# Kernel tuning notes

Measured on AMD Instinct MI355X. Metric: run time of the kernel, lower is better.

Reference implementation:

```python
import jax, jax.numpy as jnp
import numpy as np

N_HEAD = 8
D_MODEL = 128  # per-head dim == d_model in this 'interpretable' MHA
B, S = 2, 2048
LN_EPS = 1e-3  # keras LayerNormalization default epsilon


def setup_inputs() -> dict:
    key = jax.random.key(0)
    ks = jax.random.split(key, 8)
    sc = 1.0 / np.sqrt(D_MODEL)
    q = jax.random.normal(ks[0], (B, S, D_MODEL), jnp.float32)
    k = jax.random.normal(ks[1], (B, S, D_MODEL), jnp.float32)
    v = jax.random.normal(ks[2], (B, S, D_MODEL), jnp.float32)
    # multiplicative causal mask (lower-triangular ones), broadcast over B,H
    mask = jnp.tril(jnp.ones((S, S), jnp.float32))[None, None, :, :]
    Wq = jax.random.normal(ks[3], (D_MODEL, N_HEAD * D_MODEL), jnp.float32) * sc
    Wk = jax.random.normal(ks[4], (D_MODEL, N_HEAD * D_MODEL), jnp.float32) * sc
    Wv = jax.random.normal(ks[5], (D_MODEL, N_HEAD * D_MODEL), jnp.float32) * sc
    Wo = jax.random.normal(ks[6], (N_HEAD * D_MODEL, D_MODEL), jnp.float32) * sc
    gamma = jnp.ones((D_MODEL,), jnp.float32)
    beta = jnp.zeros((D_MODEL,), jnp.float32)
    return {"q": q, "k": k, "v": v, "mask": mask, "Wq": Wq, "Wk": Wk,
            "Wv": Wv, "Wo": Wo, "gamma": gamma, "beta": beta}


def reference(q, k, v, mask, Wq, Wk, Wv, Wo, gamma, beta):
    b = q.shape[0]
    # projections -> [B, H, S, D]
    def split_heads(x):
        return x.reshape(b, -1, N_HEAD, D_MODEL).transpose(0, 2, 1, 3)
    qs = split_heads(q @ Wq)
    ks_ = split_heads(k @ Wk)
    vs = split_heads(v @ Wv)
    scores = jnp.einsum('bhqd,bhkd->bhqk', qs, ks_) / jnp.sqrt(jnp.float32(D_MODEL))
    scores = scores * mask  # multiplicative mask (NOT additive -inf)
    attn = jax.nn.softmax(scores, axis=-1)
    # dropout layers are identity at inference
    out = jnp.einsum('bhqk,bhkd->bhqd', attn, vs)
    out = out.transpose(0, 2, 1, 3).reshape(b, -1, N_HEAD * D_MODEL)
    out = out @ Wo
    # keras LayerNorm (axis=-1, eps=1e-3)
    mu = jnp.mean(out, axis=-1, keepdims=True)
    var = jnp.var(out, axis=-1, keepdims=True)
    out = (out - mu) * jax.lax.rsqrt(var + LN_EPS) * gamma + beta
    return out
```

## Files before the change

kernel.cpp:

```cpp
#include <hip/hip_runtime.h>
#include <math.h>

#define B 2
#define S 2048
#define H 8
#define D 128
#define DM 1024
#define BH 16

typedef unsigned short u16;
typedef __attribute__((ext_vector_type(8))) short bf16x8;
typedef __attribute__((ext_vector_type(8))) unsigned short u16x8;
typedef __attribute__((ext_vector_type(4))) float f32x4;

__device__ __forceinline__ float bf2f(u16 x) {
    union { unsigned u; float f; } c; c.u = ((unsigned)x) << 16; return c.f;
}
__device__ __forceinline__ u16 f2bf(float f) {
    union { unsigned u; float f; } c; c.f = f;
    unsigned u = c.u; u += 0x7fffu + ((u >> 16) & 1u);
    return (u16)(u >> 16);
}
__device__ __forceinline__ u16 ftr(float f) {
    union { unsigned u; float f; } c; c.f = f;
    return (u16)(c.u >> 16);
}

#define MFMA16(a, b, c) __builtin_amdgcn_mfma_f32_16x16x32_bf16((a), (b), (c), 0, 0, 0)

__global__ __launch_bounds__(256) void proj_kernel(
    const float* __restrict__ q, const float* __restrict__ k, const float* __restrict__ v,
    const float* __restrict__ Wq, const float* __restrict__ Wk, const float* __restrict__ Wv,
    u16* __restrict__ Qo, u16* __restrict__ Ko, u16* __restrict__ VTo)
{
    __shared__ __align__(16) u16 Xs[128][136];
    __shared__ __align__(16) u16 Wst[128][136];
    int tid = threadIdx.x;
    int m0 = blockIdx.x * 128;
    int by = blockIdx.y;
    int t = by >> 3;
    int col0 = (by & 7) * 128;
    const float* X = (t == 0) ? q : (t == 1) ? k : v;
    const float* W = (t == 0) ? Wq : (t == 1) ? Wk : Wv;

    u16 (*Wtmp)[136] = Xs;
#pragma unroll
    for (int i = 0; i < 16; i++) {
        int e = i * 256 + tid; int kk = e >> 5, n4 = e & 31;
        float4 w4 = *(const float4*)&W[(size_t)kk * DM + col0 + n4 * 4];
        ushort4 p; p.x = ftr(w4.x); p.y = ftr(w4.y); p.z = ftr(w4.z); p.w = ftr(w4.w);
        *(ushort4*)&Wtmp[kk][n4 * 4] = p;
    }
    __syncthreads();
#pragma unroll
    for (int i = 0; i < 8; i++) {
        int e = i * 256 + tid; int kk = e >> 4, n8 = e & 15;
        u16x8 t8 = *(const u16x8*)&Wtmp[kk][n8 * 8];
#pragma unroll
        for (int j0 = 0; j0 < 8; j0++) {
            int j = (j0 + n8) & 7;
            Wst[n8 * 8 + j][kk] = t8[j];
        }
    }
    __syncthreads();
#pragma unroll
    for (int i = 0; i < 16; i++) {
        int e = i * 256 + tid; int r = e >> 5, c4 = e & 31;
        float4 x4 = *(const float4*)&X[(size_t)(m0 + r) * D + c4 * 4];
        ushort4 p; p.x = ftr(x4.x); p.y = ftr(x4.y); p.z = ftr(x4.z); p.w = ftr(x4.w);
        *(ushort4*)&Xs[r][c4 * 4] = p;
    }
    __syncthreads();

    int w = tid >> 6, lane = tid & 63, quad = lane >> 4, ln = lane & 15;
    bf16x8 aX[2][4];
#pragma unroll
    for (int rf = 0; rf < 2; rf++)
#pragma unroll
        for (int ks = 0; ks < 4; ks++)
            aX[rf][ks] = *(const bf16x8*)&Xs[w * 32 + rf * 16 + ln][ks * 32 + quad * 8];

    f32x4 zero = {0.f, 0.f, 0.f, 0.f};
    f32x4 acc[2][8];
#pragma unroll
    for (int rf = 0; rf < 2; rf++)
#pragma unroll
        for (int nt = 0; nt < 8; nt++) acc[rf][nt] = zero;

#pragma unroll
    for (int ks = 0; ks < 4; ks++)
#pragma unroll
        for (int nt = 0; nt < 8; nt++) {
            bf16x8 bW = *(const bf16x8*)&Wst[nt * 16 + ln][ks * 32 + quad * 8];
            acc[0][nt] = MFMA16(aX[0][ks], bW, acc[0][nt]);
            acc[1][nt] = MFMA16(aX[1][ks], bW, acc[1][nt]);
        }

    int hh = col0 >> 7, bb = m0 >> 11, ss0 = m0 & 2047;
    int bh = bb * 8 + hh;
    if (t < 2) {
        u16* O = (t == 0) ? Qo : Ko;
#pragma unroll
        for (int rf = 0; rf < 2; rf++)
#pragma unroll
            for (int nt = 0; nt < 8; nt++)
#pragma unroll
                for (int r = 0; r < 4; r++) {
                    int ss = ss0 + w * 32 + rf * 16 + quad * 4 + r;
                    O[((size_t)bh * S + ss) * D + nt * 16 + ln] = f2bf(acc[rf][nt][r]);
                }
    } else {
        __syncthreads();
        u16 (*Ct)[136] = Xs;
#pragma unroll
        for (int rf = 0; rf < 2; rf++)
#pragma unroll
            for (int nt = 0; nt < 8; nt++)
#pragma unroll
                for (int r = 0; r < 4; r++)
                    Ct[nt * 16 + ln][w * 32 + rf * 16 + quad * 4 + r] = f2bf(acc[rf][nt][r]);
        __syncthreads();
#pragma unroll
        for (int i = 0; i < 8; i++) {
            int e = i * 256 + tid; int dloc = e >> 4, s8 = e & 15;
            *(u16x8*)&VTo[((size_t)bh * D + dloc) * S + ss0 + s8 * 8] =
                *(const u16x8*)&Ct[dloc][s8 * 8];
        }
    }
}

__global__ __launch_bounds__(256) void wot_kernel(
    const float* __restrict__ Wo, u16* __restrict__ WoT)
{
    __shared__ __align__(16) u16 Wl[64][136];
    int tid = threadIdx.x, k0 = blockIdx.x * 64;
#pragma unroll
    for (int i = 0; i < 8; i++) {
        int e = i * 256 + tid; int kk = e >> 5, n4 = e & 31;
        float4 w4 = *(const float4*)&Wo[(size_t)(k0 + kk) * D + n4 * 4];
        ushort4 p; p.x = ftr(w4.x); p.y = ftr(w4.y); p.z = ftr(w4.z); p.w = ftr(w4.w);
        *(ushort4*)&Wl[kk][n4 * 4] = p;
    }
    __syncthreads();
    int n = tid >> 1, kh = tid & 1;
    u16 tmp[32];
#pragma unroll
    for (int j = 0; j < 32; j++) tmp[j] = Wl[kh * 32 + j][n];
#pragma unroll
    for (int j8 = 0; j8 < 4; j8++)
        *(u16x8*)&WoT[(size_t)n * DM + k0 + kh * 32 + j8 * 8] = *(const u16x8*)&tmp[j8 * 8];
}

__global__ __launch_bounds__(128) void chunk_sum_kernel(
    const u16* __restrict__ VT, float* __restrict__ Csum)
{
    int bh = blockIdx.x, c = blockIdx.y, d = threadIdx.x;
    const u16* p = VT + ((size_t)bh * D + d) * S + c * 64;
    float acc = 0.f;
#pragma unroll
    for (int i = 0; i < 8; i++) {
        u16x8 v8 = *(const u16x8*)&p[i * 8];
#pragma unroll
        for (int j = 0; j < 8; j++) acc += bf2f(v8[j]);
    }
    Csum[((size_t)bh * 32 + c) * D + d] = acc;
}

__global__ __launch_bounds__(128) void scan_kernel(
    const float* __restrict__ Csum, float* __restrict__ SufT)
{
    int bh = blockIdx.x, d = threadIdx.x;
    float acc = 0.f;
    for (int c = 31; c >= 0; c--) {
        SufT[((size_t)bh * 32 + c) * D + d] = acc;
        acc += Csum[((size_t)bh * 32 + c) * D + d];
    }
}

__global__ __launch_bounds__(512, 2) void attn_kernel(
    const u16* __restrict__ Qb, const u16* __restrict__ Kb, const u16* __restrict__ VTg,
    const float* __restrict__ SufT, u16* __restrict__ HOb)
{
    __shared__ __align__(16) u16 Qs[2][64][136];
    __shared__ __align__(16) u16 Ks[128][136];
    __shared__ __align__(16) u16 Vt[128][136];
    __shared__ __align__(16) u16 Ps[2][64][136];
    __shared__ float Lred[2][4][64];

    int tid = threadIdx.x;
    int bx = blockIdx.x, bh = blockIdx.y;
    int nhi = (31 - bx) / 2 + 1, nlo = bx / 2 + 1;
    int w = tid >> 6, qt = w >> 2, wq = w & 3, lane = tid & 63, quad = lane >> 4, ln = lane & 15;
    int qb = qt ? bx : (31 - bx);
    int q0 = qb * 64;
    int nq = qt ? nlo : nhi;
    const u16* Qp  = Qb  + (size_t)bh * S * D;
    const u16* Kp  = Kb  + (size_t)bh * S * D;
    const u16* VTp = VTg + (size_t)bh * D * S;

#pragma unroll
    for (int i = 0; i < 4; i++) {
        int e = i * 512 + tid; int r2 = e >> 4, c8 = e & 15;
        int qtt = r2 >> 6, r = r2 & 63;
        int q0s = (qtt ? bx : (31 - bx)) * 64;
        *(u16x8*)&Qs[qtt][r][c8 * 8] = *(const u16x8*)&Qp[(size_t)(q0s + r) * D + c8 * 8];
    }
    __syncthreads();
    bf16x8 aQ[4][4];
#pragma unroll
    for (int rf = 0; rf < 4; rf++)
#pragma unroll
        for (int ks = 0; ks < 4; ks++)
            aQ[rf][ks] = *(const bf16x8*)&Qs[qt][rf * 16 + ln][ks * 32 + quad * 8];

    f32x4 zero = {0.f, 0.f, 0.f, 0.f};
    f32x4 accPV[4][2], acc_l[4];
#pragma unroll
    for (int rf = 0; rf < 4; rf++) { accPV[rf][0] = zero; accPV[rf][1] = zero; acc_l[rf] = zero; }
    bf16x8 bOnes;
#pragma unroll
    for (int j = 0; j < 8; j++) bOnes[j] = (short)0x3F80;
    const float scale = 0.08838834764831845f;

    for (int kt = 0; kt < nhi; kt++) {
        __syncthreads();
        int k0 = kt * 128;
#pragma unroll
        for (int i = 0; i < 4; i++) {
            int e = i * 512 + tid; int r = e >> 4, c8 = e & 15;
            *(u16x8*)&Ks[r][c8 * 8] = *(const u16x8*)&Kp[(size_t)(k0 + r) * D + c8 * 8];
        }
#pragma unroll
        for (int i = 0; i < 4; i++) {
            int e = i * 512 + tid; int dd = e >> 4, c8 = e & 15;
            *(u16x8*)&Vt[dd][c8 * 8] = *(const u16x8*)&VTp[(size_t)dd * S + k0 + c8 * 8];
        }
        __syncthreads();
        bool active = (qt == 0) || (kt < nlo);
        if (active) {
            f32x4 s[4][2];
#pragma unroll
            for (int rf = 0; rf < 4; rf++) { s[rf][0] = zero; s[rf][1] = zero; }
#pragma unroll
            for (int ks = 0; ks < 4; ks++) {
                bf16x8 b0 = *(const bf16x8*)&Ks[wq * 32 + ln][ks * 32 + quad * 8];
                bf16x8 b1 = *(const bf16x8*)&Ks[wq * 32 + 16 + ln][ks * 32 + quad * 8];
#pragma unroll
                for (int rf = 0; rf < 4; rf++) {
                    s[rf][0] = MFMA16(aQ[rf][ks], b0, s[rf][0]);
                    s[rf][1] = MFMA16(aQ[rf][ks], b1, s[rf][1]);
                }
            }
#pragma unroll
            for (int rf = 0; rf < 4; rf++)
#pragma unroll
                for (int ct = 0; ct < 2; ct++) {
                    int col = k0 + wq * 32 + ct * 16 + ln;
                    int rowb = q0 + rf * 16 + quad * 4;
#pragma unroll
                    for (int r = 0; r < 4; r++) {
                        float tv = (col <= rowb + r) ? s[rf][ct][r] : 0.f;
                        float p = __expf(tv * scale);
                        Ps[qt][rf * 16 + quad * 4 + r][wq * 32 + ct * 16 + ln] = f2bf(p);
                    }
                }
        }
        __syncthreads();
        if (active) {
#pragma unroll
            for (int ks = 0; ks < 4; ks++) {
                bf16x8 aP[4];
#pragma unroll
                for (int rf = 0; rf < 4; rf++)
                    aP[rf] = *(const bf16x8*)&Ps[qt][rf * 16 + ln][ks * 32 + quad * 8];
                bf16x8 v0 = *(const bf16x8*)&Vt[wq * 32 + ln][ks * 32 + quad * 8];
                bf16x8 v1 = *(const bf16x8*)&Vt[wq * 32 + 16 + ln][ks * 32 + quad * 8];
                if (ks == wq) {
#pragma unroll
                    for (int rf = 0; rf < 4; rf++) acc_l[rf] = MFMA16(aP[rf], bOnes, acc_l[rf]);
                }
#pragma unroll
                for (int rf = 0; rf < 4; rf++) {
                    accPV[rf][0] = MFMA16(aP[rf], v0, accPV[rf][0]);
                    accPV[rf][1] = MFMA16(aP[rf], v1, accPV[rf][1]);
                }
            }
        }
    }

    __syncthreads();
    if (ln == 0) {
#pragma unroll
        for (int rf = 0; rf < 4; rf++)
#pragma unroll
            for (int r = 0; r < 4; r++)
                Lred[qt][wq][rf * 16 + quad * 4 + r] = acc_l[rf][r];
    }
    __syncthreads();

    int scount = S - nq * 128;
    size_t sufb = (size_t)(bh * 32 + 2 * nq - 1) * D + wq * 32;
    float suf0 = SufT[sufb + ln];
    float suf1 = SufT[sufb + 16 + ln];
    int b = bh >> 3, h = bh & 7;
#pragma unroll
    for (int rf = 0; rf < 4; rf++)
#pragma unroll
        for (int r = 0; r < 4; r++) {
            int row = rf * 16 + quad * 4 + r;
            int srow = q0 + row;
            float l = Lred[qt][0][row] + Lred[qt][1][row] + Lred[qt][2][row] + Lred[qt][3][row]
                      + (float)scount;
            float inv = 1.f / l;
            size_t base = ((size_t)(b * S + srow)) * DM + h * D + wq * 32;
            HOb[base + ln]      = f2bf((accPV[rf][0][r] + suf0) * inv);
            HOb[base + 16 + ln] = f2bf((accPV[rf][1][r] + suf1) * inv);
        }
}

__global__ __launch_bounds__(256) void out_ln_kernel(
    const u16* __restrict__ HOb, const u16* __restrict__ WoT,
    const float* __restrict__ gamma, const float* __restrict__ beta,
    float* __restrict__ out)
{
    __shared__ __align__(16) u16 HOs[16][1048];
    __shared__ float Cs[16][132];
    int tid = threadIdx.x;
    int m0 = blockIdx.x * 16;
    int w = tid >> 6, lane = tid & 63, quad = lane >> 4, ln = lane & 15;
#pragma unroll
    for (int i = 0; i < 8; i++) {
        int e = i * 256 + tid; int r = e >> 7, c8 = e & 127;
        *(u16x8*)&HOs[r][c8 * 8] = *(const u16x8*)&HOb[(size_t)(m0 + r) * DM + c8 * 8];
    }
    __syncthreads();
    f32x4 zero = {0.f, 0.f, 0.f, 0.f};
    f32x4 acc[2] = {zero, zero};
#pragma unroll 4
    for (int ks = 0; ks < 32; ks++) {
        bf16x8 aH = *(const bf16x8*)&HOs[ln][ks * 32 + quad * 8];
        bf16x8 w0 = *(const bf16x8*)&WoT[(size_t)(w * 32 + ln) * DM + ks * 32 + quad * 8];
        bf16x8 w1 = *(const bf16x8*)&WoT[(size_t)(w * 32 + 16 + ln) * DM + ks * 32 + quad * 8];
        acc[0] = MFMA16(aH, w0, acc[0]);
        acc[1] = MFMA16(aH, w1, acc[1]);
    }
#pragma unroll
    for (int ct = 0; ct < 2; ct++)
#pragma unroll
        for (int r = 0; r < 4; r++)
            Cs[quad * 4 + r][w * 32 + ct * 16 + ln] = acc[ct][r];
    __syncthreads();

    int row = tid >> 4, t16 = tid & 15;
    float xv[8], sum = 0.f, sq = 0.f;
#pragma unroll
    for (int j = 0; j < 8; j++) {
        float x = Cs[row][t16 * 8 + j];
        xv[j] = x; sum += x; sq += x * x;
    }
#pragma unroll
    for (int off = 1; off < 16; off <<= 1) {
        sum += __shfl_xor(sum, off);
        sq  += __shfl_xor(sq, off);
    }
    float mu = sum * (1.f / 128.f);
    float var = sq * (1.f / 128.f) - mu * mu;
    float rstd = rsqrtf(var + 1e-3f);
    float o[8];
#pragma unroll
    for (int j = 0; j < 8; j++) {
        int c = t16 * 8 + j;
        o[j] = (xv[j] - mu) * rstd * gamma[c] + beta[c];
    }
    float* op = &out[(size_t)(m0 + row) * D + t16 * 8];
    *(float4*)&op[0] = *(float4*)&o[0];
    *(float4*)&op[4] = *(float4*)&o[4];
}

extern "C" void kernel_launch(void* const* d_in, const int* in_sizes, int n_in,
                              void* d_out, int out_size, void* d_ws, size_t ws_size,
                              hipStream_t stream)
{
    const float* q     = (const float*)d_in[0];
    const float* k     = (const float*)d_in[1];
    const float* v     = (const float*)d_in[2];
    const float* Wq    = (const float*)d_in[4];
    const float* Wk    = (const float*)d_in[5];
    const float* Wv    = (const float*)d_in[6];
    const float* Wo    = (const float*)d_in[7];
    const float* gamma = (const float*)d_in[8];
    const float* beta  = (const float*)d_in[9];

    u16* ws16 = (u16*)d_ws;
    u16* Qb  = ws16;
    u16* Kb  = ws16 + 4194304;
    u16* VT  = ws16 + 8388608;
    u16* HOb = ws16 + 12582912;
    u16* WoT = ws16 + 16777216;
    float* Csum = (float*)((char*)d_ws + 33816576);
    float* SufT = (float*)((char*)d_ws + 34078720);

    wot_kernel<<<16, 256, 0, stream>>>(Wo, WoT);
    proj_kernel<<<dim3(32, 24), 256, 0, stream>>>(q, k, v, Wq, Wk, Wv, Qb, Kb, VT);
    chunk_sum_kernel<<<dim3(BH, 32), 128, 0, stream>>>(VT, Csum);
    scan_kernel<<<BH, 128, 0, stream>>>(Csum, SufT);
    attn_kernel<<<dim3(16, BH), 512, 0, stream>>>(Qb, Kb, VT, SufT, HOb);
    out_ln_kernel<<<256, 256, 0, stream>>>(HOb, WoT, gamma, beta, (float*)d_out);
}
```

Measured before the change: 161.6 us.

## Pretranspose projection weights once and fuse chunk sums into projection kernel

A new prep kernel converts Wq/Wk/Wv to bf16 and transposes them once into global workspace, replacing the Wo-only transpose kernel. Each of the 768 projection blocks then reads its pre-transposed weight tile from global memory instead of rebuilding it in shared memory. The per-64-row V chunk sums are computed in the V projection epilogue from the shared-memory tile, removing the separate chunk_sum kernel launch and its re-read of VT. The cost is loading B-operand fragments straight from global/L2 memory inside the MFMA loop rather than from LDS.

```diff
diff --git a/kernel.cpp b/kernel.cpp
--- a/kernel.cpp
+++ b/kernel.cpp
@@ -28,41 +28,70 @@
 
 #define MFMA16(a, b, c) __builtin_amdgcn_mfma_f32_16x16x32_bf16((a), (b), (c), 0, 0, 0)
 
+__global__ __launch_bounds__(256) void prep_kernel(
+    const float* __restrict__ Wq, const float* __restrict__ Wk, const float* __restrict__ Wv,
+    const float* __restrict__ Wo, u16* __restrict__ WT, u16* __restrict__ WoT)
+{
+    __shared__ __align__(16) u16 Wl[128][132];
+    int tid = threadIdx.x, by = blockIdx.x;
+    if (by < 16) {
+        int k0 = by * 64;
+#pragma unroll
+        for (int i = 0; i < 8; i++) {
+            int e = i * 256 + tid; int kk = e >> 5, n4 = e & 31;
+            float4 w4 = *(const float4*)&Wo[(size_t)(k0 + kk) * D + n4 * 4];
+            ushort4 p; p.x = ftr(w4.x); p.y = ftr(w4.y); p.z = ftr(w4.z); p.w = ftr(w4.w);
+            *(ushort4*)&Wl[kk][n4 * 4] = p;
+        }
+        __syncthreads();
+#pragma unroll
+        for (int i = 0; i < 4; i++) {
+            int e = i * 256 + tid; int n = e >> 3, ko = e & 7;
+            u16x8 g;
+#pragma unroll
+            for (int j = 0; j < 8; j++) g[j] = Wl[ko * 8 + j][n];
+            *(u16x8*)&WoT[(size_t)n * DM + k0 + ko * 8] = g;
+        }
+    } else {
+        int tile = by - 16;
+        int t = tile >> 3, h = tile & 7;
+        const float* W = (t == 0) ? Wq : (t == 1) ? Wk : Wv;
+        int col0 = h * 128;
+#pragma unroll
+        for (int i = 0; i < 16; i++) {
+            int e = i * 256 + tid; int kk = e >> 5, n4 = e & 31;
+            float4 w4 = *(const float4*)&W[(size_t)kk * DM + col0 + n4 * 4];
+            ushort4 p; p.x = ftr(w4.x); p.y = ftr(w4.y); p.z = ftr(w4.z); p.w = ftr(w4.w);
+            *(ushort4*)&Wl[kk][n4 * 4] = p;
+        }
+        __syncthreads();
+        u16* WTt = WT + (size_t)tile * (128 * 128);
+#pragma unroll
+        for (int i = 0; i < 8; i++) {
+            int e = i * 256 + tid; int n = e >> 4, ko = e & 15;
+            u16x8 g;
+#pragma unroll
+            for (int j = 0; j < 8; j++) g[j] = Wl[ko * 8 + j][n];
+            *(u16x8*)&WTt[(size_t)n * 128 + ko * 8] = g;
+        }
+    }
+}
+
 __global__ __launch_bounds__(256) void proj_kernel(
     const float* __restrict__ q, const float* __restrict__ k, const float* __restrict__ v,
-    const float* __restrict__ Wq, const float* __restrict__ Wk, const float* __restrict__ Wv,
-    u16* __restrict__ Qo, u16* __restrict__ Ko, u16* __restrict__ VTo)
+    const u16* __restrict__ WT,
+    u16* __restrict__ Qo, u16* __restrict__ Ko, u16* __restrict__ VTo,
+    float* __restrict__ Csum)
 {
     __shared__ __align__(16) u16 Xs[128][136];
-    __shared__ __align__(16) u16 Wst[128][136];
     int tid = threadIdx.x;
     int m0 = blockIdx.x * 128;
     int by = blockIdx.y;
     int t = by >> 3;
-    int col0 = (by & 7) * 128;
+    int h = by & 7;
     const float* X = (t == 0) ? q : (t == 1) ? k : v;
-    const float* W = (t == 0) ? Wq : (t == 1) ? Wk : Wv;
-
-    u16 (*Wtmp)[136] = Xs;
-#pragma unroll
-    for (int i = 0; i < 16; i++) {
-        int e = i * 256 + tid; int kk = e >> 5, n4 = e & 31;
-        float4 w4 = *(const float4*)&W[(size_t)kk * DM + col0 + n4 * 4];
-        ushort4 p; p.x = ftr(w4.x); p.y = ftr(w4.y); p.z = ftr(w4.z); p.w = ftr(w4.w);
-        *(ushort4*)&Wtmp[kk][n4 * 4] = p;
-    }
-    __syncthreads();
-#pragma unroll
-    for (int i = 0; i < 8; i++) {
-        int e = i * 256 + tid; int kk = e >> 4, n8 = e & 15;
-        u16x8 t8 = *(const u16x8*)&Wtmp[kk][n8 * 8];
-#pragma unroll
-        for (int j0 = 0; j0 < 8; j0++) {
-            int j = (j0 + n8) & 7;
-            Wst[n8 * 8 + j][kk] = t8[j];
-        }
-    }
-    __syncthreads();
+    const u16* WTt = WT + (size_t)(t * 8 + h) * (128 * 128);
+
 #pragma unroll
     for (int i = 0; i < 16; i++) {
         int e = i * 256 + tid; int r = e >> 5, c4 = e & 31;
@@ -88,16 +117,20 @@
         for (int nt = 0; nt < 8; nt++) acc[rf][nt] = zero;
 
 #pragma unroll
-    for (int ks = 0; ks < 4; ks++)
+    for (int ks = 0; ks < 4; ks++) {
+        bf16x8 bW[8];
+#pragma unroll
+        for (int nt = 0; nt < 8; nt++)
+            bW[nt] = *(const bf16x8*)&WTt[(size_t)(nt * 16 + ln) * 128 + ks * 32 + quad * 8];
 #pragma unroll
         for (int nt = 0; nt < 8; nt++) {
-            bf16x8 bW = *(const bf16x8*)&Wst[nt * 16 + ln][ks * 32 + quad * 8];
-            acc[0][nt] = MFMA16(aX[0][ks], bW, acc[0][nt]);
-            acc[1][nt] = MFMA16(aX[1][ks], bW, acc[1][nt]);
-        }
-
-    int hh = col0 >> 7, bb = m0 >> 11, ss0 = m0 & 2047;
-    int bh = bb * 8 + hh;
+            acc[0][nt] = MFMA16(aX[0][ks], bW[nt], acc[0][nt]);
+            acc[1][nt] = MFMA16(aX[1][ks], bW[nt], acc[1][nt]);
+        }
+    }
+
+    int bb = m0 >> 11, ss0 = m0 & 2047;
+    int bh = bb * 8 + h;
     if (t < 2) {
         u16* O = (t == 0) ? Qo : Ko;
 #pragma unroll
@@ -126,44 +159,18 @@
             *(u16x8*)&VTo[((size_t)bh * D + dloc) * S + ss0 + s8 * 8] =
                 *(const u16x8*)&Ct[dloc][s8 * 8];
         }
-    }
-}
-
-__global__ __launch_bounds__(256) void wot_kernel(
-    const float* __restrict__ Wo, u16* __restrict__ WoT)
-{
-    __shared__ __align__(16) u16 Wl[64][136];
-    int tid = threadIdx.x, k0 = blockIdx.x * 64;
-#pragma unroll
-    for (int i = 0; i < 8; i++) {
-        int e = i * 256 + tid; int kk = e >> 5, n4 = e & 31;
-        float4 w4 = *(const float4*)&Wo[(size_t)(k0 + kk) * D + n4 * 4];
-        ushort4 p; p.x = ftr(w4.x); p.y = ftr(w4.y); p.z = ftr(w4.z); p.w = ftr(w4.w);
-        *(ushort4*)&Wl[kk][n4 * 4] = p;
-    }
-    __syncthreads();
-    int n = tid >> 1, kh = tid & 1;
-    u16 tmp[32];
-#pragma unroll
-    for (int j = 0; j < 32; j++) tmp[j] = Wl[kh * 32 + j][n];
-#pragma unroll
-    for (int j8 = 0; j8 < 4; j8++)
-        *(u16x8*)&WoT[(size_t)n * DM + k0 + kh * 32 + j8 * 8] = *(const u16x8*)&tmp[j8 * 8];
-}
-
-__global__ __launch_bounds__(128) void chunk_sum_kernel(
-    const u16* __restrict__ VT, float* __restrict__ Csum)
-{
-    int bh = blockIdx.x, c = blockIdx.y, d = threadIdx.x;
-    const u16* p = VT + ((size_t)bh * D + d) * S + c * 64;
-    float acc = 0.f;
-#pragma unroll
-    for (int i = 0; i < 8; i++) {
-        u16x8 v8 = *(const u16x8*)&p[i * 8];
-#pragma unroll
-        for (int j = 0; j < 8; j++) acc += bf2f(v8[j]);
-    }
-    Csum[((size_t)bh * 32 + c) * D + d] = acc;
+        {
+            int d = tid >> 1, c = tid & 1;
+            float s = 0.f;
+#pragma unroll
+            for (int i = 0; i < 8; i++) {
+                u16x8 v8 = *(const u16x8*)&Ct[d][c * 64 + i * 8];
+#pragma unroll
+                for (int j = 0; j < 8; j++) s += bf2f(v8[j]);
+            }
+            Csum[((size_t)bh * 32 + (ss0 >> 6) + c) * D + d] = s;
+        }
+    }
 }
 
 __global__ __launch_bounds__(128) void scan_kernel(
@@ -397,12 +404,12 @@
     u16* VT  = ws16 + 8388608;
     u16* HOb = ws16 + 12582912;
     u16* WoT = ws16 + 16777216;
-    float* Csum = (float*)((char*)d_ws + 33816576);
-    float* SufT = (float*)((char*)d_ws + 34078720);
-
-    wot_kernel<<<16, 256, 0, stream>>>(Wo, WoT);
-    proj_kernel<<<dim3(32, 24), 256, 0, stream>>>(q, k, v, Wq, Wk, Wv, Qb, Kb, VT);
-    chunk_sum_kernel<<<dim3(BH, 32), 128, 0, stream>>>(VT, Csum);
+    u16* WT  = ws16 + 16908288;
+    float* Csum = (float*)((char*)d_ws + 35651584);
+    float* SufT = (float*)((char*)d_ws + 35913728);
+
+    prep_kernel<<<40, 256, 0, stream>>>(Wq, Wk, Wv, Wo, WT, WoT);
+    proj_kernel<<<dim3(32, 24), 256, 0, stream>>>(q, k, v, WT, Qb, Kb, VT, Csum);
     scan_kernel<<<BH, 128, 0, stream>>>(Csum, SufT);
     attn_kernel<<<dim3(16, BH), 512, 0, stream>>>(Qb, Kb, VT, SufT, HOb);
     out_ln_kernel<<<256, 256, 0, stream>>>(HOb, WoT, gamma, beta, (float*)d_out);
```

After: 165.4 us. 1.02x slower.
